# Performance work log

Hardware: AMD Instinct MI355X
Metric: run time of the kernel (lower is better)

Reference implementation:

```python
import jax, jax.numpy as jnp
import numpy as np

B, T, F, U, M = 4096, 16, 256, 512, 8
DELTA_T = 0.04

# ln_tau_table: tau = 1, 10^0.5, 10^1.0, ... -> ln(tau) = i * 0.5*ln(10)
LN_TAU = (jnp.arange(M, dtype=jnp.float32) * (0.5 * np.log(10.0))).astype(jnp.float32)
DECAY = jnp.exp(-DELTA_T / (LN_TAU + 1e-7))  # [M]


def setup_inputs() -> dict:
    key = jax.random.key(0)
    ks = jax.random.split(key, 9)
    s = lambda fan_in: 1.0 / np.sqrt(fan_in)
    return {
        "x": jax.random.normal(ks[0], (B, T, F), dtype=jnp.float32),
        "W_r": jax.random.normal(ks[1], (F + U, U * M), dtype=jnp.float32) * s(F + U),
        "b_r": jax.random.normal(ks[2], (U * M,), dtype=jnp.float32) * 0.01,
        "W_q": jax.random.normal(ks[3], (F + U, U), dtype=jnp.float32) * s(F + U),
        "b_q": jax.random.normal(ks[4], (U,), dtype=jnp.float32) * 0.01,
        "W_s": jax.random.normal(ks[5], (F + U, U * M), dtype=jnp.float32) * s(F + U),
        "b_s": jax.random.normal(ks[6], (U * M,), dtype=jnp.float32) * 0.01,
        "W_out": jax.random.normal(ks[7], (U, 3), dtype=jnp.float32) * s(U),
        "b_out": jax.random.normal(ks[8], (3,), dtype=jnp.float32) * 0.01,
    }


def _ctgru_forward(x, W_r, b_r, W_q, b_q, W_s, b_s, W_out, b_out):
    def step(h_hat, x_t):  # h_hat: [B,U,M], x_t: [B,F]
        h = h_hat.sum(axis=2)                              # [B,U]
        fused = jnp.concatenate([x_t, h], axis=1)          # [B,F+U]
        ln_tau_r = (fused @ W_r + b_r).reshape(-1, U, M)   # [B,U,M]
        r_ki = jax.nn.softmax(-jnp.square(ln_tau_r - LN_TAU), axis=2)
        q_in = jnp.concatenate([x_t, jnp.sum(r_ki * h_hat, axis=2)], axis=1)
        q_k = jnp.tanh(q_in @ W_q + b_q)[:, :, None]       # [B,U,1]
        ln_tau_s = (fused @ W_s + b_s).reshape(-1, U, M)
        s_ki = jax.nn.softmax(-jnp.square(ln_tau_s - LN_TAU), axis=2)
        h_next = ((1.0 - s_ki) * h_hat + s_ki * q_k) * DECAY
        return h_next, h_next.sum(axis=2)                  # carry, hidden [B,U]

    h0 = jnp.zeros((x.shape[0], U, M), dtype=x.dtype)
    _, hiddens = jax.lax.scan(step, h0, jnp.swapaxes(x, 0, 1))  # hiddens: [T,B,U]
    outputs = jnp.swapaxes(hiddens, 0, 1)                  # [B,T,U]
    return outputs @ W_out + b_out                         # [B,T,3]


def reference(x, W_r, b_r, W_q, b_q, W_s, b_s, W_out, b_out):
    return _ctgru_forward(x, W_r, b_r, W_q, b_q, W_s, b_s, W_out, b_out)
```

## Files before the change

kernel.cpp:

```cpp
#include <hip/hip_runtime.h>
#include <hip/hip_bf16.h>
#include <math.h>

#define B_   4096
#define T_   16
#define F_   256
#define U_   512
#define M_   8
#define K_   768
#define NRS  4096
#define NC   8192
#define LNT  1.1512925f

#define XPH  32768
#define XPT  1048576
#define HPH  65536
#define BPH  98304
#define QPH  49152

typedef __bf16 bf16_t;
typedef bf16_t bf16x8 __attribute__((ext_vector_type(8)));
typedef bf16_t bf16x4 __attribute__((ext_vector_type(4)));
typedef float  f32x4  __attribute__((ext_vector_type(4)));

__device__ inline void gl_lds16(const void* g, void* lds) {
    __builtin_amdgcn_global_load_lds(
        (const __attribute__((address_space(1))) unsigned int*)g,
        (__attribute__((address_space(3))) unsigned int*)lds, 16, 0, 0);
}

#define VMCNT(n) asm volatile("s_waitcnt vmcnt(" #n ")" ::: "memory")
#define LGKM0()  asm volatile("s_waitcnt lgkmcnt(0)" ::: "memory")
#define BAR()    __builtin_amdgcn_s_barrier()

__device__ inline void stage8(const bf16_t* src, bf16_t* dst, int tid) {
    gl_lds16(src + tid * 8,        (char*)dst + tid * 16);
    gl_lds16(src + tid * 8 + 2048, (char*)dst + tid * 16 + 4096);
}

template <int IS_R>
__global__ __launch_bounds__(256, 4) void gemm_half(
    const bf16_t* __restrict__ xt_t,
    const bf16_t* __restrict__ ht,
    const bf16_t* __restrict__ Bt,
    const float*  __restrict__ biasP,
    const bf16_t* __restrict__ hhat,
    bf16_t* __restrict__ rh,
    bf16_t* __restrict__ sbuf)
{
    __shared__ __attribute__((aligned(16))) bf16_t Ahl[2][4096];
    __shared__ __attribute__((aligned(16))) bf16_t Bhl[2][4096];

    const int tid  = threadIdx.x;
    const int lane = tid & 63;
    const int wave = tid >> 6;

    const int lin = blockIdx.y * 32 + blockIdx.x;
    const int c = lin & 7, q = lin >> 3;
    const int mh = (c >> 1) * 8 + (q & 7);
    const int nh = (c & 1) * 16 + (q >> 3);
    const int m0 = mh * 128;
    const int NH = IS_R ? nh : 32 + nh;

    const int wm = wave >> 1;
    const int wn = wave & 1;
    const int lr = lane & 15;
    const int kq = lane >> 4;

    const bf16_t* xp = xt_t + (size_t)mh * XPH;
    const bf16_t* hp = ht   + (size_t)mh * HPH;
    const bf16_t* bp = Bt   + (size_t)NH * BPH;

    const int aoff = kq * 1024 + (wm * 64 + lr) * 8;
    const int boff = kq * 1024 + (wn * 64 + lr) * 8;

    f32x4 acc[4][4] = {};

    stage8(xp, &Ahl[0][0], tid);
    stage8(bp, &Bhl[0][0], tid);
    VMCNT(0);
    BAR();

#pragma unroll
    for (int tt = 0; tt < 24; ++tt) {
        const int p = tt & 1, pn = p ^ 1;
        if (tt < 23) {
            const bf16_t* as = (tt + 1 < 8) ? xp + (tt + 1) * 4096
                                            : hp + (tt + 1 - 8) * 4096;
            stage8(as, &Ahl[pn][0], tid);
            stage8(bp + (tt + 1) * 4096, &Bhl[pn][0], tid);
        }
        bf16x8 a[4], b[4];
#pragma unroll
        for (int i = 0; i < 4; ++i)
            a[i] = *(const bf16x8*)(&Ahl[p][0] + aoff + i * 128);
#pragma unroll
        for (int j = 0; j < 4; ++j)
            b[j] = *(const bf16x8*)(&Bhl[p][0] + boff + j * 128);
        LGKM0();
        __builtin_amdgcn_s_setprio(1);
#pragma unroll
        for (int i = 0; i < 4; ++i)
#pragma unroll
            for (int j = 0; j < 4; ++j)
                acc[i][j] = __builtin_amdgcn_mfma_f32_16x16x32_bf16(
                    a[i], b[j], acc[i][j], 0, 0, 0);
        __builtin_amdgcn_s_setprio(0);
        VMCNT(0);
        BAR();
    }

    const int nb  = NH * 128 + wn * 64;
    const int u3  = lane & 7;
    const int m0v = ((lane >> 3) & 1) * 4;

    float bj4[4];
#pragma unroll
    for (int j = 0; j < 4; ++j) bj4[j] = biasP[nb + j * 16 + lr];

#pragma unroll
    for (int mi = 0; mi < 4; ++mi) {
        const int rowb = m0 + wm * 64 + mi * 16 + kq * 4;
#pragma unroll
        for (int r = 0; r < 4; ++r) {
            const int row = rowb + r;
            float e[4], sum = 0.f;
#pragma unroll
            for (int j = 0; j < 4; ++j) {
                float v = acc[mi][j][r] + bj4[j];
                float d = v - (float)(m0v + j) * LNT;
                e[j] = __expf(-d * d);
                sum += e[j];
            }
            sum += __shfl_xor(sum, 8, 64);
            const float inv = 1.0f / sum;
            if (IS_R) {
                bf16x4 h4 = *(const bf16x4*)(hhat + (size_t)row * NRS + nb + u3 * 8 + m0v);
                float rhv = 0.f;
#pragma unroll
                for (int j = 0; j < 4; ++j) rhv += e[j] * inv * (float)h4[j];
                rhv += __shfl_xor(rhv, 8, 64);
                if ((lane & 8) == 0)
                    rh[(size_t)row * U_ + (nb >> 3) + u3] = (bf16_t)rhv;
            } else {
                bf16x4 pv;
#pragma unroll
                for (int j = 0; j < 4; ++j) pv[j] = (bf16_t)(e[j] * inv);
                *(bf16x4*)(sbuf + (size_t)row * NRS + (nb - NRS) + u3 * 8 + m0v) = pv;
            }
        }
    }
}

__global__ __launch_bounds__(256) void gemm_q_up(
    const bf16_t* __restrict__ xt_t,
    const bf16_t* __restrict__ rh,
    const bf16_t* __restrict__ Bqt,
    const float*  __restrict__ bq,
    const bf16_t* __restrict__ sbuf,
    bf16_t* __restrict__ hhat,
    bf16_t* __restrict__ hnext,
    bf16_t* __restrict__ htile)
{
    __shared__ __attribute__((aligned(16))) bf16_t As[4096];
    __shared__ __attribute__((aligned(16))) bf16_t Bs[4096];

    const int tid  = threadIdx.x;
    const int lane = tid & 63;
    const int wave = tid >> 6;
    const int m0 = blockIdx.x * 64;
    const int n0 = blockIdx.y * 64;
    const int wm = wave & 1;
    const int wn = wave >> 1;
    const int lr = lane & 15;
    const int kq = lane >> 4;

    const int chs = (tid >> 6) & 3;
    const int rws = tid & 63;

    const bf16_t* xp  = xt_t + (size_t)(m0 >> 7) * XPH;
    const int     r0  = m0 & 127;
    const bf16_t* bpq = Bqt + (size_t)(n0 >> 6) * QPH;

    f32x4 acc[2][2] = {};

    for (int kt = 0; kt < 12; ++kt) {
        __syncthreads();
        if (kt < 4) {
            gl_lds16(xp + ((size_t)((kt * 2 + 0) * 4 + chs) * 128 + r0 + rws) * 8,
                     (char*)As + tid * 16);
            gl_lds16(xp + ((size_t)((kt * 2 + 1) * 4 + chs) * 128 + r0 + rws) * 8,
                     (char*)As + tid * 16 + 4096);
        } else {
            const int cb = (kt - 4) * 64;
            gl_lds16(rh + (size_t)(m0 + rws) * U_ + cb + chs * 8,
                     (char*)As + tid * 16);
            gl_lds16(rh + (size_t)(m0 + rws) * U_ + cb + 32 + chs * 8,
                     (char*)As + tid * 16 + 4096);
        }
        gl_lds16(bpq + ((size_t)((kt * 2 + 0) * 4 + chs) * 64 + rws) * 8,
                 (char*)Bs + tid * 16);
        gl_lds16(bpq + ((size_t)((kt * 2 + 1) * 4 + chs) * 64 + rws) * 8,
                 (char*)Bs + tid * 16 + 4096);
        __syncthreads();

        bf16x8 af[4], bfr[4];
#pragma unroll
        for (int ks = 0; ks < 2; ks++)
#pragma unroll
            for (int i = 0; i < 2; i++) {
                af[i * 2 + ks]  = *(const bf16x8*)(As +
                    ((ks * 4 + kq) * 64 + wm * 32 + i * 16 + lr) * 8);
                bfr[i * 2 + ks] = *(const bf16x8*)(Bs +
                    ((ks * 4 + kq) * 64 + wn * 32 + i * 16 + lr) * 8);
            }
#pragma unroll
        for (int ks = 0; ks < 2; ks++)
#pragma unroll
            for (int i = 0; i < 2; i++)
#pragma unroll
                for (int j = 0; j < 2; j++)
                    acc[i][j] = __builtin_amdgcn_mfma_f32_16x16x32_bf16(
                        af[i * 2 + ks], bfr[j * 2 + ks], acc[i][j], 0, 0, 0);
    }

    const float DEC[8] = {0.0f, 0.9658531f, 0.9827783f, 0.9884856f,
                          0.9913518f, 0.9930754f, 0.9942261f, 0.9950489f};

#pragma unroll
    for (int i = 0; i < 2; i++) {
        const int rowb = m0 + wm * 32 + i * 16 + kq * 4;
#pragma unroll
        for (int j = 0; j < 2; j++) {
            const int u = n0 + wn * 32 + j * 16 + lr;
            const float bv = bq[u];
#pragma unroll
            for (int r = 0; r < 4; r++) {
                const int row = rowb + r;
                const float qv = tanhf(acc[i][j][r] + bv);
                const size_t base = (size_t)row * NRS + u * 8;
                bf16x8 s8 = *(const bf16x8*)(sbuf + base);
                bf16x8 h8 = *(const bf16x8*)(hhat + base);
                bf16x8 ho;
                float hs = 0.f;
#pragma unroll
                for (int m = 0; m < 8; m++) {
                    float s = (float)s8[m];
                    float h = (float)h8[m];
                    float hn = ((1.f - s) * h + s * qv) * DEC[m];
                    ho[m] = (bf16_t)hn;
                    hs += hn;
                }
                *(bf16x8*)(hhat + base) = ho;
                hnext[(size_t)row * U_ + u] = (bf16_t)hs;
                htile[((size_t)(row >> 7) * 16 + (u >> 5)) * 4096
                      + ((((u >> 3) & 3) * 128) + (row & 127)) * 8 + (u & 7)] = (bf16_t)hs;
            }
        }
    }
}

__global__ void transpose_perm(const float* __restrict__ src, bf16_t* __restrict__ dst) {
    __shared__ float tl[32][33];
    int k0 = blockIdx.x * 32, n0 = blockIdx.y * 32;
    int tx = threadIdx.x & 31, ty = threadIdx.x >> 5;
#pragma unroll
    for (int i = 0; i < 32; i += 8)
        tl[ty + i][tx] = src[(size_t)(k0 + ty + i) * NRS + n0 + tx];
    __syncthreads();
#pragma unroll
    for (int i = 0; i < 32; i += 8) {
        int n = n0 + ty + i;
        int m = n & 7, u3v = (n >> 3) & 7;
        int p = (n & ~63) + (m & 3) * 16 + (m >> 2) * 8 + u3v;
        dst[(size_t)p * K_ + k0 + tx] = (bf16_t)tl[tx][ty + i];
    }
}

__global__ void btile_build(const bf16_t* __restrict__ WrsT, bf16_t* __restrict__ Bt) {
    int n = blockIdx.x / 3;
    int k = (blockIdx.x % 3) * 256 + threadIdx.x;
    int NH = n >> 7, prow = n & 127;
    int kt = k >> 5, ch = (k >> 3) & 3, e = k & 7;
    Bt[(size_t)NH * BPH + (((size_t)kt * 4 + ch) * 128 + prow) * 8 + e]
        = WrsT[(size_t)n * K_ + k];
}

__global__ void transpose_plain(const float* __restrict__ src, bf16_t* __restrict__ dst, int N) {
    __shared__ float tl[32][33];
    int k0 = blockIdx.x * 32, n0 = blockIdx.y * 32;
    int tx = threadIdx.x & 31, ty = threadIdx.x >> 5;
#pragma unroll
    for (int i = 0; i < 32; i += 8)
        tl[ty + i][tx] = src[(size_t)(k0 + ty + i) * N + n0 + tx];
    __syncthreads();
#pragma unroll
    for (int i = 0; i < 32; i += 8)
        dst[(size_t)(n0 + ty + i) * K_ + k0 + tx] = (bf16_t)tl[tx][ty + i];
}

__global__ void bqtile_build(const bf16_t* __restrict__ WqT, bf16_t* __restrict__ Bqt) {
    int n = blockIdx.x / 3;
    int k = (blockIdx.x % 3) * 256 + threadIdx.x;
    int np = n >> 6, prow = n & 63;
    int kt = k >> 5, ch = (k >> 3) & 3, e = k & 7;
    Bqt[(size_t)np * QPH + (((size_t)kt * 4 + ch) * 64 + prow) * 8 + e]
        = WqT[(size_t)n * K_ + k];
}

__global__ void bias_perm(const float* __restrict__ b_r, const float* __restrict__ b_s,
                          float* __restrict__ biasP) {
    int p = blockIdx.x * 256 + threadIdx.x;
    int pr = p & 63, j = pr >> 4, lr = pr & 15;
    int L = (p & ~63) + (lr & 7) * 8 + ((lr >> 3) & 1) * 4 + j;
    biasP[p] = (L < NRS) ? b_r[L] : b_s[L - NRS];
}

__global__ void xtile_build(const float* __restrict__ x, bf16_t* __restrict__ xt) {
    int idx = blockIdx.x * 256 + threadIdx.x;
    int b = idx >> 12;
    int rem = idx & 4095;
    int t = rem >> 8, f = rem & 255;
    int mh = b >> 7, prow = b & 127;
    int kt = f >> 5, ch = (f >> 3) & 3, e = f & 7;
    xt[(size_t)t * XPT + (size_t)mh * XPH
       + (((size_t)kt * 4 + ch) * 128 + prow) * 8 + e] = (bf16_t)x[idx];
}

__global__ __launch_bounds__(256) void out_all(
    const bf16_t* __restrict__ hall,
    const float* __restrict__ Wout,
    const float* __restrict__ bout,
    float* __restrict__ out)
{
    int row = blockIdx.x * 4 + (threadIdx.x >> 6);
    int lane = threadIdx.x & 63;
    bf16x8 h8 = *(const bf16x8*)(hall + (size_t)row * U_ + lane * 8);
    float p0 = 0, p1 = 0, p2 = 0;
#pragma unroll
    for (int k = 0; k < 8; k++) {
        float h = (float)h8[k];
        int u = lane * 8 + k;
        p0 += h * Wout[u * 3 + 0];
        p1 += h * Wout[u * 3 + 1];
        p2 += h * Wout[u * 3 + 2];
    }
    for (int off = 32; off; off >>= 1) {
        p0 += __shfl_down(p0, off, 64);
        p1 += __shfl_down(p1, off, 64);
        p2 += __shfl_down(p2, off, 64);
    }
    if (lane == 0) {
        int t = row >> 12, b = row & (B_ - 1);
        size_t o = ((size_t)b * T_ + t) * 3;
        out[o + 0] = p0 + bout[0];
        out[o + 1] = p1 + bout[1];
        out[o + 2] = p2 + bout[2];
    }
}

extern "C" void kernel_launch(void* const* d_in, const int* in_sizes, int n_in,
                              void* d_out, int out_size, void* d_ws, size_t ws_size,
                              hipStream_t stream) {
    const float* x   = (const float*)d_in[0];
    const float* W_r = (const float*)d_in[1];
    const float* b_r = (const float*)d_in[2];
    const float* W_q = (const float*)d_in[3];
    const float* b_q = (const float*)d_in[4];
    const float* W_s = (const float*)d_in[5];
    const float* b_s = (const float*)d_in[6];
    const float* W_o = (const float*)d_in[7];
    const float* b_o = (const float*)d_in[8];
    float* out = (float*)d_out;

    char* ws = (char*)d_ws;
    bf16_t* hhat  = (bf16_t*)ws; ws += (size_t)B_ * NRS * 2;
    bf16_t* sbuf  = (bf16_t*)ws; ws += (size_t)B_ * NRS * 2;
    bf16_t* xtile = (bf16_t*)ws; ws += (size_t)T_ * XPT * 2;
    bf16_t* hall  = (bf16_t*)ws; ws += (size_t)(T_ + 1) * B_ * U_ * 2;
    bf16_t* rh    = (bf16_t*)ws; ws += (size_t)B_ * U_ * 2;
    bf16_t* WrsT  = (bf16_t*)ws; ws += (size_t)NC * K_ * 2;
    bf16_t* Btile = (bf16_t*)ws; ws += (size_t)NC * K_ * 2;
    bf16_t* htile = (bf16_t*)ws; ws += (size_t)32 * HPH * 2;
    bf16_t* WqT   = (bf16_t*)ws; ws += (size_t)U_ * K_ * 2;
    bf16_t* Bqtil = (bf16_t*)ws; ws += (size_t)8 * QPH * 2;
    float*  biasP = (float*)ws;  ws += (size_t)NC * 4;

    hipMemsetAsync(hhat, 0, (size_t)B_ * NRS * 2, stream);
    hipMemsetAsync(htile, 0, (size_t)32 * HPH * 2, stream);
    xtile_build<<<B_ * T_ * F_ / 256, 256, 0, stream>>>(x, xtile);
    transpose_perm<<<dim3(K_ / 32, NRS / 32), 256, 0, stream>>>(W_r, WrsT);
    transpose_perm<<<dim3(K_ / 32, NRS / 32), 256, 0, stream>>>(W_s, WrsT + (size_t)NRS * K_);
    btile_build<<<NC * 3, 256, 0, stream>>>(WrsT, Btile);
    transpose_plain<<<dim3(K_ / 32, U_ / 32), 256, 0, stream>>>(W_q, WqT, U_);
    bqtile_build<<<U_ * 3, 256, 0, stream>>>(WqT, Bqtil);
    bias_perm<<<NC / 256, 256, 0, stream>>>(b_r, b_s, biasP);

    for (int t = 0; t < T_; t++) {
        const bf16_t* xt_t = xtile + (size_t)t * XPT;
        bf16_t*       hn   = hall + (size_t)(t + 1) * B_ * U_;
        gemm_half<1><<<dim3(32, 32), 256, 0, stream>>>(xt_t, htile, Btile, biasP, hhat, rh, sbuf);
        gemm_half<0><<<dim3(32, 32), 256, 0, stream>>>(xt_t, htile, Btile, biasP, hhat, rh, sbuf);
        gemm_q_up<<<dim3(64, 8), 256, 0, stream>>>(xt_t, rh, Bqtil, b_q, sbuf, hhat, hn, htile);
    }
    out_all<<<B_ * T_ / 4, 256, 0, stream>>>(hall + (size_t)B_ * U_, W_o, b_o, out);
}
```

Baseline: 1.496 ms.

## Merge r/s GEMMs into one launch loading fragments directly from global

```diff
diff --git a/kernel.cpp b/kernel.cpp
--- a/kernel.cpp
+++ b/kernel.cpp
@@ -29,17 +29,7 @@
         (__attribute__((address_space(3))) unsigned int*)lds, 16, 0, 0);
 }
 
-#define VMCNT(n) asm volatile("s_waitcnt vmcnt(" #n ")" ::: "memory")
-#define LGKM0()  asm volatile("s_waitcnt lgkmcnt(0)" ::: "memory")
-#define BAR()    __builtin_amdgcn_s_barrier()
-
-__device__ inline void stage8(const bf16_t* src, bf16_t* dst, int tid) {
-    gl_lds16(src + tid * 8,        (char*)dst + tid * 16);
-    gl_lds16(src + tid * 8 + 2048, (char*)dst + tid * 16 + 4096);
-}
-
-template <int IS_R>
-__global__ __launch_bounds__(256, 4) void gemm_half(
+__global__ __launch_bounds__(256) void gemm_rs_fd(
     const bf16_t* __restrict__ xt_t,
     const bf16_t* __restrict__ ht,
     const bf16_t* __restrict__ Bt,
@@ -48,71 +38,62 @@
     bf16_t* __restrict__ rh,
     bf16_t* __restrict__ sbuf)
 {
-    __shared__ __attribute__((aligned(16))) bf16_t Ahl[2][4096];
-    __shared__ __attribute__((aligned(16))) bf16_t Bhl[2][4096];
-
     const int tid  = threadIdx.x;
     const int lane = tid & 63;
     const int wave = tid >> 6;
 
     const int lin = blockIdx.y * 32 + blockIdx.x;
     const int c = lin & 7, q = lin >> 3;
-    const int mh = (c >> 1) * 8 + (q & 7);
-    const int nh = (c & 1) * 16 + (q >> 3);
+    const int mh = (c >> 2) * 16 + (q & 15);
+    const int NH = (c & 3) * 16 + (q >> 4);
     const int m0 = mh * 128;
-    const int NH = IS_R ? nh : 32 + nh;
 
     const int wm = wave >> 1;
     const int wn = wave & 1;
     const int lr = lane & 15;
     const int kq = lane >> 4;
 
-    const bf16_t* xp = xt_t + (size_t)mh * XPH;
-    const bf16_t* hp = ht   + (size_t)mh * HPH;
-    const bf16_t* bp = Bt   + (size_t)NH * BPH;
+    const bf16_t* apx = xt_t + (size_t)mh * XPH;
+    const bf16_t* aph = ht   + (size_t)mh * HPH;
+    const bf16_t* bp  = Bt   + (size_t)NH * BPH;
 
     const int aoff = kq * 1024 + (wm * 64 + lr) * 8;
     const int boff = kq * 1024 + (wn * 64 + lr) * 8;
 
     f32x4 acc[4][4] = {};
-
-    stage8(xp, &Ahl[0][0], tid);
-    stage8(bp, &Bhl[0][0], tid);
-    VMCNT(0);
-    BAR();
-
-#pragma unroll
-    for (int tt = 0; tt < 24; ++tt) {
-        const int p = tt & 1, pn = p ^ 1;
-        if (tt < 23) {
-            const bf16_t* as = (tt + 1 < 8) ? xp + (tt + 1) * 4096
-                                            : hp + (tt + 1 - 8) * 4096;
-            stage8(as, &Ahl[pn][0], tid);
-            stage8(bp + (tt + 1) * 4096, &Bhl[pn][0], tid);
-        }
-        bf16x8 a[4], b[4];
-#pragma unroll
-        for (int i = 0; i < 4; ++i)
-            a[i] = *(const bf16x8*)(&Ahl[p][0] + aoff + i * 128);
-#pragma unroll
-        for (int j = 0; j < 4; ++j)
-            b[j] = *(const bf16x8*)(&Bhl[p][0] + boff + j * 128);
-        LGKM0();
-        __builtin_amdgcn_s_setprio(1);
-#pragma unroll
-        for (int i = 0; i < 4; ++i)
-#pragma unroll
-            for (int j = 0; j < 4; ++j)
-                acc[i][j] = __builtin_amdgcn_mfma_f32_16x16x32_bf16(
-                    a[i], b[j], acc[i][j], 0, 0, 0);
-        __builtin_amdgcn_s_setprio(0);
-        VMCNT(0);
-        BAR();
-    }
+    bf16x8 a0[4], b0[4], a1[4], b1[4];
+
+#define ABASE(T) ((T) < 8 ? apx + (T) * 4096 : aph + ((T) - 8) * 4096)
+#define LDA(D, T) do{ const bf16_t* _p = ABASE(T) + aoff;                      \
+    D[0] = *(const bf16x8*)(_p);        D[1] = *(const bf16x8*)(_p + 128);     \
+    D[2] = *(const bf16x8*)(_p + 256);  D[3] = *(const bf16x8*)(_p + 384); }while(0)
+#define LDB(D, T) do{ const bf16_t* _p = bp + (T) * 4096 + boff;               \
+    D[0] = *(const bf16x8*)(_p);        D[1] = *(const bf16x8*)(_p + 128);     \
+    D[2] = *(const bf16x8*)(_p + 256);  D[3] = *(const bf16x8*)(_p + 384); }while(0)
+#define MMA(A, B) do{ __builtin_amdgcn_s_setprio(1);                           \
+    _Pragma("unroll") for (int i = 0; i < 4; ++i)                              \
+      _Pragma("unroll") for (int j = 0; j < 4; ++j)                            \
+        acc[i][j] = __builtin_amdgcn_mfma_f32_16x16x32_bf16(                   \
+            A[i], B[j], acc[i][j], 0, 0, 0);                                   \
+    __builtin_amdgcn_s_setprio(0); }while(0)
+
+    LDA(a0, 0); LDB(b0, 0);
+#pragma unroll
+    for (int tt = 0; tt < 24; tt += 2) {
+        if (tt + 1 < 24) { LDA(a1, tt + 1); LDB(b1, tt + 1); }
+        MMA(a0, b0);
+        if (tt + 2 < 24) { LDA(a0, tt + 2); LDB(b0, tt + 2); }
+        MMA(a1, b1);
+    }
+#undef MMA
+#undef LDB
+#undef LDA
+#undef ABASE
 
     const int nb  = NH * 128 + wn * 64;
     const int u3  = lane & 7;
     const int m0v = ((lane >> 3) & 1) * 4;
+    const bool is_r = NH < 32;
 
     float bj4[4];
 #pragma unroll
@@ -134,7 +115,7 @@
             }
             sum += __shfl_xor(sum, 8, 64);
             const float inv = 1.0f / sum;
-            if (IS_R) {
+            if (is_r) {
                 bf16x4 h4 = *(const bf16x4*)(hhat + (size_t)row * NRS + nb + u3 * 8 + m0v);
                 float rhv = 0.f;
 #pragma unroll
@@ -318,13 +299,20 @@
 
 __global__ void xtile_build(const float* __restrict__ x, bf16_t* __restrict__ xt) {
     int idx = blockIdx.x * 256 + threadIdx.x;
-    int b = idx >> 12;
-    int rem = idx & 4095;
-    int t = rem >> 8, f = rem & 255;
+    int b = idx >> 9;
+    int rem = idx & 511;
+    int t = rem >> 5, c8 = rem & 31;
+    int f0 = c8 * 8;
+    const float* src = x + ((size_t)b * T_ + t) * F_ + f0;
+    float4 v0 = *(const float4*)(src);
+    float4 v1 = *(const float4*)(src + 4);
+    bf16x8 o;
+    o[0] = (bf16_t)v0.x; o[1] = (bf16_t)v0.y; o[2] = (bf16_t)v0.z; o[3] = (bf16_t)v0.w;
+    o[4] = (bf16_t)v1.x; o[5] = (bf16_t)v1.y; o[6] = (bf16_t)v1.z; o[7] = (bf16_t)v1.w;
     int mh = b >> 7, prow = b & 127;
-    int kt = f >> 5, ch = (f >> 3) & 3, e = f & 7;
-    xt[(size_t)t * XPT + (size_t)mh * XPH
-       + (((size_t)kt * 4 + ch) * 128 + prow) * 8 + e] = (bf16_t)x[idx];
+    int kt = f0 >> 5, ch = (f0 >> 3) & 3;
+    *(bf16x8*)(xt + (size_t)t * XPT + (size_t)mh * XPH
+               + (((size_t)kt * 4 + ch) * 128 + prow) * 8) = o;
 }
 
 __global__ __launch_bounds__(256) void out_all(
@@ -388,7 +376,7 @@
 
     hipMemsetAsync(hhat, 0, (size_t)B_ * NRS * 2, stream);
     hipMemsetAsync(htile, 0, (size_t)32 * HPH * 2, stream);
-    xtile_build<<<B_ * T_ * F_ / 256, 256, 0, stream>>>(x, xtile);
+    xtile_build<<<B_ * T_ * F_ / 8 / 256, 256, 0, stream>>>(x, xtile);
     transpose_perm<<<dim3(K_ / 32, NRS / 32), 256, 0, stream>>>(W_r, WrsT);
     transpose_perm<<<dim3(K_ / 32, NRS / 32), 256, 0, stream>>>(W_s, WrsT + (size_t)NRS * K_);
     btile_build<<<NC * 3, 256, 0, stream>>>(WrsT, Btile);
@@ -399,8 +387,7 @@
     for (int t = 0; t < T_; t++) {
         const bf16_t* xt_t = xtile + (size_t)t * XPT;
         bf16_t*       hn   = hall + (size_t)(t + 1) * B_ * U_;
-        gemm_half<1><<<dim3(32, 32), 256, 0, stream>>>(xt_t, htile, Btile, biasP, hhat, rh, sbuf);
-        gemm_half<0><<<dim3(32, 32), 256, 0, stream>>>(xt_t, htile, Btile, biasP, hhat, rh, sbuf);
+        gemm_rs_fd<<<dim3(32, 64), 256, 0, stream>>>(xt_t, htile, Btile, biasP, hhat, rh, sbuf);
         gemm_q_up<<<dim3(64, 8), 256, 0, stream>>>(xt_t, rh, Bqtil, b_q, sbuf, hhat, hn, htile);
     }
     out_all<<<B_ * T_ / 4, 256, 0, stream>>>(hall + (size_t)B_ * U_, W_o, b_o, out);
```

Result: slower. 1.823 ms (+21.8%).

## Fuse s-gate GEMM with q-gate GEMM and state update; skip h-part at t=0

Applied to the files above, without the earlier changes.

```diff
diff --git a/kernel.cpp b/kernel.cpp
--- a/kernel.cpp
+++ b/kernel.cpp
@@ -16,7 +16,7 @@
 #define XPT  1048576
 #define HPH  65536
 #define BPH  98304
-#define QPH  49152
+#define QPP  12288
 
 typedef __bf16 bf16_t;
 typedef bf16_t bf16x8 __attribute__((ext_vector_type(8)));
@@ -38,15 +38,13 @@
     gl_lds16(src + tid * 8 + 2048, (char*)dst + tid * 16 + 4096);
 }
 
-template <int IS_R>
-__global__ __launch_bounds__(256, 4) void gemm_half(
+__global__ __launch_bounds__(256, 4) void gemm_r(
     const bf16_t* __restrict__ xt_t,
     const bf16_t* __restrict__ ht,
     const bf16_t* __restrict__ Bt,
     const float*  __restrict__ biasP,
     const bf16_t* __restrict__ hhat,
-    bf16_t* __restrict__ rh,
-    bf16_t* __restrict__ sbuf)
+    bf16_t* __restrict__ rh)
 {
     __shared__ __attribute__((aligned(16))) bf16_t Ahl[2][4096];
     __shared__ __attribute__((aligned(16))) bf16_t Bhl[2][4096];
@@ -60,7 +58,7 @@
     const int mh = (c >> 1) * 8 + (q & 7);
     const int nh = (c & 1) * 16 + (q >> 3);
     const int m0 = mh * 128;
-    const int NH = IS_R ? nh : 32 + nh;
+    const int NH = nh;
 
     const int wm = wave >> 1;
     const int wn = wave & 1;
@@ -134,127 +132,202 @@
             }
             sum += __shfl_xor(sum, 8, 64);
             const float inv = 1.0f / sum;
-            if (IS_R) {
-                bf16x4 h4 = *(const bf16x4*)(hhat + (size_t)row * NRS + nb + u3 * 8 + m0v);
-                float rhv = 0.f;
-#pragma unroll
-                for (int j = 0; j < 4; ++j) rhv += e[j] * inv * (float)h4[j];
-                rhv += __shfl_xor(rhv, 8, 64);
-                if ((lane & 8) == 0)
-                    rh[(size_t)row * U_ + (nb >> 3) + u3] = (bf16_t)rhv;
-            } else {
-                bf16x4 pv;
-#pragma unroll
-                for (int j = 0; j < 4; ++j) pv[j] = (bf16_t)(e[j] * inv);
-                *(bf16x4*)(sbuf + (size_t)row * NRS + (nb - NRS) + u3 * 8 + m0v) = pv;
-            }
-        }
-    }
-}
-
-__global__ __launch_bounds__(256) void gemm_q_up(
+            bf16x4 h4 = *(const bf16x4*)(hhat + (size_t)row * NRS + nb + u3 * 8 + m0v);
+            float rhv = 0.f;
+#pragma unroll
+            for (int j = 0; j < 4; ++j) rhv += e[j] * inv * (float)h4[j];
+            rhv += __shfl_xor(rhv, 8, 64);
+            if ((lane & 8) == 0)
+                rh[(size_t)row * U_ + (nb >> 3) + u3] = (bf16_t)rhv;
+        }
+    }
+}
+
+template <int FIRST>
+__global__ __launch_bounds__(256, 4) void gemm_sq(
     const bf16_t* __restrict__ xt_t,
+    const bf16_t* __restrict__ htr,
+    const bf16_t* __restrict__ Bt,
+    const float*  __restrict__ biasP,
     const bf16_t* __restrict__ rh,
-    const bf16_t* __restrict__ Bqt,
+    const bf16_t* __restrict__ Bq16,
     const float*  __restrict__ bq,
-    const bf16_t* __restrict__ sbuf,
     bf16_t* __restrict__ hhat,
     bf16_t* __restrict__ hnext,
-    bf16_t* __restrict__ htile)
+    bf16_t* __restrict__ htw)
 {
-    __shared__ __attribute__((aligned(16))) bf16_t As[4096];
-    __shared__ __attribute__((aligned(16))) bf16_t Bs[4096];
+    __shared__ __attribute__((aligned(16))) bf16_t Ahl[2][4096];
+    __shared__ __attribute__((aligned(16))) bf16_t Bhl[2][4096];
+    __shared__ __attribute__((aligned(16))) float  qls[2048];
 
     const int tid  = threadIdx.x;
     const int lane = tid & 63;
     const int wave = tid >> 6;
-    const int m0 = blockIdx.x * 64;
-    const int n0 = blockIdx.y * 64;
-    const int wm = wave & 1;
-    const int wn = wave >> 1;
+
+    const int lin = blockIdx.y * 32 + blockIdx.x;
+    const int c = lin & 7, qq = lin >> 3;
+    const int mh = (c >> 1) * 8 + (qq & 7);
+    const int nh = (c & 1) * 16 + (qq >> 3);
+    const int m0 = mh * 128;
+    const int NH = 32 + nh;
+
+    const int wm = wave >> 1;
+    const int wn = wave & 1;
     const int lr = lane & 15;
     const int kq = lane >> 4;
 
-    const int chs = (tid >> 6) & 3;
-    const int rws = tid & 63;
-
-    const bf16_t* xp  = xt_t + (size_t)(m0 >> 7) * XPH;
-    const int     r0  = m0 & 127;
-    const bf16_t* bpq = Bqt + (size_t)(n0 >> 6) * QPH;
-
-    f32x4 acc[2][2] = {};
-
-    for (int kt = 0; kt < 12; ++kt) {
-        __syncthreads();
-        if (kt < 4) {
-            gl_lds16(xp + ((size_t)((kt * 2 + 0) * 4 + chs) * 128 + r0 + rws) * 8,
-                     (char*)As + tid * 16);
-            gl_lds16(xp + ((size_t)((kt * 2 + 1) * 4 + chs) * 128 + r0 + rws) * 8,
-                     (char*)As + tid * 16 + 4096);
-        } else {
-            const int cb = (kt - 4) * 64;
-            gl_lds16(rh + (size_t)(m0 + rws) * U_ + cb + chs * 8,
-                     (char*)As + tid * 16);
-            gl_lds16(rh + (size_t)(m0 + rws) * U_ + cb + 32 + chs * 8,
-                     (char*)As + tid * 16 + 4096);
-        }
-        gl_lds16(bpq + ((size_t)((kt * 2 + 0) * 4 + chs) * 64 + rws) * 8,
-                 (char*)Bs + tid * 16);
-        gl_lds16(bpq + ((size_t)((kt * 2 + 1) * 4 + chs) * 64 + rws) * 8,
-                 (char*)Bs + tid * 16 + 4096);
-        __syncthreads();
-
-        bf16x8 af[4], bfr[4];
-#pragma unroll
-        for (int ks = 0; ks < 2; ks++)
-#pragma unroll
-            for (int i = 0; i < 2; i++) {
-                af[i * 2 + ks]  = *(const bf16x8*)(As +
-                    ((ks * 4 + kq) * 64 + wm * 32 + i * 16 + lr) * 8);
-                bfr[i * 2 + ks] = *(const bf16x8*)(Bs +
-                    ((ks * 4 + kq) * 64 + wn * 32 + i * 16 + lr) * 8);
+    const bf16_t* xp = xt_t + (size_t)mh * XPH;
+    const bf16_t* hp = htr  + (size_t)mh * HPH;
+    const bf16_t* bp = Bt   + (size_t)NH * BPH;
+    const bf16_t* bqp = Bq16 + (size_t)nh * QPP;
+
+    const int NT = FIRST ? 8 : 24;
+
+    {
+        bf16_t* bslab = &Bhl[0][0];
+        f32x4 accq[2] = {};
+
+        const int rws = tid & 127, chs = tid >> 7;
+
+#define STAGE_AQ(KT, DST) do{                                                  \
+        if ((KT) < 8) stage8(xp + (KT) * 4096, DST, tid);                      \
+        else {                                                                 \
+            const int cb_ = ((KT) - 8) * 32;                                   \
+            gl_lds16(rh + (size_t)(m0 + rws) * U_ + cb_ + chs * 8,             \
+                     (char*)(DST) + tid * 16);                                 \
+            gl_lds16(rh + (size_t)(m0 + rws) * U_ + cb_ + 16 + chs * 8,        \
+                     (char*)(DST) + tid * 16 + 4096);                          \
+        } }while(0)
+#define STAGE_BQ(KT, P) do{ if (wave == 0)                                     \
+        gl_lds16(bqp + (KT) * 512 + lane * 8,                                  \
+                 (char*)bslab + (P) * 1024 + lane * 16); }while(0)
+
+        STAGE_AQ(0, &Ahl[0][0]);
+        STAGE_BQ(0, 0);
+        VMCNT(0);
+        BAR();
+#pragma unroll
+        for (int kt = 0; kt < NT; ++kt) {
+            const int p = kt & 1, pn = p ^ 1;
+            if (kt < NT - 1) { STAGE_AQ(kt + 1, &Ahl[pn][0]); STAGE_BQ(kt + 1, pn); }
+            bf16x8 aq[2], bqf;
+#pragma unroll
+            for (int i = 0; i < 2; ++i)
+                aq[i] = *(const bf16x8*)(&Ahl[p][0] + kq * 1024
+                                         + (wave * 32 + i * 16 + lr) * 8);
+            bqf = *(const bf16x8*)(bslab + p * 512 + (kq * 16 + lr) * 8);
+            LGKM0();
+#pragma unroll
+            for (int i = 0; i < 2; ++i)
+                accq[i] = __builtin_amdgcn_mfma_f32_16x16x32_bf16(
+                    aq[i], bqf, accq[i], 0, 0, 0);
+            VMCNT(0);
+            BAR();
+        }
+#undef STAGE_AQ
+#undef STAGE_BQ
+
+        const float bqv = bq[nh * 16 + lr];
+#pragma unroll
+        for (int i = 0; i < 2; ++i)
+#pragma unroll
+            for (int r = 0; r < 4; ++r)
+                qls[(wave * 32 + i * 16 + kq * 4 + r) * 16 + lr] =
+                    tanhf(accq[i][r] + bqv);
+        BAR();
+    }
+
+    const int aoff = kq * 1024 + (wm * 64 + lr) * 8;
+    const int boff = kq * 1024 + (wn * 64 + lr) * 8;
+
+    f32x4 acc[4][4] = {};
+
+    stage8(xp, &Ahl[0][0], tid);
+    stage8(bp, &Bhl[0][0], tid);
+    VMCNT(0);
+    BAR();
+
+#pragma unroll
+    for (int tt = 0; tt < NT; ++tt) {
+        const int p = tt & 1, pn = p ^ 1;
+        if (tt < NT - 1) {
+            const bf16_t* as = (tt + 1 < 8) ? xp + (tt + 1) * 4096
+                                            : hp + (tt + 1 - 8) * 4096;
+            stage8(as, &Ahl[pn][0], tid);
+            stage8(bp + (tt + 1) * 4096, &Bhl[pn][0], tid);
+        }
+        bf16x8 a[4], b[4];
+#pragma unroll
+        for (int i = 0; i < 4; ++i)
+            a[i] = *(const bf16x8*)(&Ahl[p][0] + aoff + i * 128);
+#pragma unroll
+        for (int j = 0; j < 4; ++j)
+            b[j] = *(const bf16x8*)(&Bhl[p][0] + boff + j * 128);
+        LGKM0();
+        __builtin_amdgcn_s_setprio(1);
+#pragma unroll
+        for (int i = 0; i < 4; ++i)
+#pragma unroll
+            for (int j = 0; j < 4; ++j)
+                acc[i][j] = __builtin_amdgcn_mfma_f32_16x16x32_bf16(
+                    a[i], b[j], acc[i][j], 0, 0, 0);
+        __builtin_amdgcn_s_setprio(0);
+        VMCNT(0);
+        BAR();
+    }
+
+    const int nb  = NH * 128 + wn * 64;
+    const int u3  = lane & 7;
+    const int m0v = ((lane >> 3) & 1) * 4;
+    const int hcol = nh * 128 + wn * 64;
+
+    const float DECL[4] = {0.0f, 0.9658531f, 0.9827783f, 0.9884856f};
+    const float DECH[4] = {0.9913518f, 0.9930754f, 0.9942261f, 0.9950489f};
+
+    float bj4[4];
+#pragma unroll
+    for (int j = 0; j < 4; ++j) bj4[j] = biasP[nb + j * 16 + lr];
+
+#pragma unroll
+    for (int mi = 0; mi < 4; ++mi) {
+        const int rowb = m0 + wm * 64 + mi * 16 + kq * 4;
+        const int rlb  = wm * 64 + mi * 16 + kq * 4;
+#pragma unroll
+        for (int r = 0; r < 4; ++r) {
+            const int row = rowb + r;
+            float e[4], sum = 0.f;
+#pragma unroll
+            for (int j = 0; j < 4; ++j) {
+                float v = acc[mi][j][r] + bj4[j];
+                float d = v - (float)(m0v + j) * LNT;
+                e[j] = __expf(-d * d);
+                sum += e[j];
             }
-#pragma unroll
-        for (int ks = 0; ks < 2; ks++)
-#pragma unroll
-            for (int i = 0; i < 2; i++)
-#pragma unroll
-                for (int j = 0; j < 2; j++)
-                    acc[i][j] = __builtin_amdgcn_mfma_f32_16x16x32_bf16(
-                        af[i * 2 + ks], bfr[j * 2 + ks], acc[i][j], 0, 0, 0);
-    }
-
-    const float DEC[8] = {0.0f, 0.9658531f, 0.9827783f, 0.9884856f,
-                          0.9913518f, 0.9930754f, 0.9942261f, 0.9950489f};
-
-#pragma unroll
-    for (int i = 0; i < 2; i++) {
-        const int rowb = m0 + wm * 32 + i * 16 + kq * 4;
-#pragma unroll
-        for (int j = 0; j < 2; j++) {
-            const int u = n0 + wn * 32 + j * 16 + lr;
-            const float bv = bq[u];
-#pragma unroll
-            for (int r = 0; r < 4; r++) {
-                const int row = rowb + r;
-                const float qv = tanhf(acc[i][j][r] + bv);
-                const size_t base = (size_t)row * NRS + u * 8;
-                bf16x8 s8 = *(const bf16x8*)(sbuf + base);
-                bf16x8 h8 = *(const bf16x8*)(hhat + base);
-                bf16x8 ho;
-                float hs = 0.f;
-#pragma unroll
-                for (int m = 0; m < 8; m++) {
-                    float s = (float)s8[m];
-                    float h = (float)h8[m];
-                    float hn = ((1.f - s) * h + s * qv) * DEC[m];
-                    ho[m] = (bf16_t)hn;
-                    hs += hn;
-                }
-                *(bf16x8*)(hhat + base) = ho;
+            sum += __shfl_xor(sum, 8, 64);
+            const float inv = 1.0f / sum;
+            const float qv = qls[(rlb + r) * 16 + wn * 8 + u3];
+
+            const size_t ha = (size_t)row * NRS + hcol + u3 * 8 + m0v;
+            bf16x4 h4;
+            if (!FIRST) h4 = *(const bf16x4*)(hhat + ha);
+            bf16x4 ho;
+            float hs = 0.f;
+#pragma unroll
+            for (int j = 0; j < 4; ++j) {
+                float s = e[j] * inv;
+                float h = FIRST ? 0.f : (float)h4[j];
+                float dec = m0v ? DECH[j] : DECL[j];
+                float hn = ((1.f - s) * h + s * qv) * dec;
+                ho[j] = (bf16_t)hn;
+                hs += hn;
+            }
+            *(bf16x4*)(hhat + ha) = ho;
+            hs += __shfl_xor(hs, 8, 64);
+            if ((lane & 8) == 0) {
+                const int u = nh * 16 + wn * 8 + u3;
                 hnext[(size_t)row * U_ + u] = (bf16_t)hs;
-                htile[((size_t)(row >> 7) * 16 + (u >> 5)) * 4096
-                      + ((((u >> 3) & 3) * 128) + (row & 127)) * 8 + (u & 7)] = (bf16_t)hs;
+                htw[((size_t)(row >> 7) * 16 + (u >> 5)) * 4096
+                    + ((((u >> 3) & 3) * 128) + (row & 127)) * 8 + (u & 7)] = (bf16_t)hs;
             }
         }
     }
@@ -286,26 +359,12 @@
         = WrsT[(size_t)n * K_ + k];
 }
 
-__global__ void transpose_plain(const float* __restrict__ src, bf16_t* __restrict__ dst, int N) {
-    __shared__ float tl[32][33];
-    int k0 = blockIdx.x * 32, n0 = blockIdx.y * 32;
-    int tx = threadIdx.x & 31, ty = threadIdx.x >> 5;
-#pragma unroll
-    for (int i = 0; i < 32; i += 8)
-        tl[ty + i][tx] = src[(size_t)(k0 + ty + i) * N + n0 + tx];
-    __syncthreads();
-#pragma unroll
-    for (int i = 0; i < 32; i += 8)
-        dst[(size_t)(n0 + ty + i) * K_ + k0 + tx] = (bf16_t)tl[tx][ty + i];
-}
-
-__global__ void bqtile_build(const bf16_t* __restrict__ WqT, bf16_t* __restrict__ Bqt) {
-    int n = blockIdx.x / 3;
-    int k = (blockIdx.x % 3) * 256 + threadIdx.x;
-    int np = n >> 6, prow = n & 63;
+__global__ void bq16_build(const float* __restrict__ Wq, bf16_t* __restrict__ Bq16) {
+    int i = blockIdx.x * 256 + threadIdx.x;
+    int k = i >> 9, u = i & 511;
+    int nh = u >> 4, ul = u & 15;
     int kt = k >> 5, ch = (k >> 3) & 3, e = k & 7;
-    Bqt[(size_t)np * QPH + (((size_t)kt * 4 + ch) * 64 + prow) * 8 + e]
-        = WqT[(size_t)n * K_ + k];
+    Bq16[(size_t)nh * QPP + ((size_t)kt * 4 + ch) * 128 + ul * 8 + e] = (bf16_t)Wq[i];
 }
 
 __global__ void bias_perm(const float* __restrict__ b_r, const float* __restrict__ b_s,
@@ -318,13 +377,20 @@
 
 __global__ void xtile_build(const float* __restrict__ x, bf16_t* __restrict__ xt) {
     int idx = blockIdx.x * 256 + threadIdx.x;
-    int b = idx >> 12;
-    int rem = idx & 4095;
-    int t = rem >> 8, f = rem & 255;
+    int b = idx >> 9;
+    int rem = idx & 511;
+    int t = rem >> 5, c8 = rem & 31;
+    int f0 = c8 * 8;
+    const float* src = x + ((size_t)b * T_ + t) * F_ + f0;
+    float4 v0 = *(const float4*)(src);
+    float4 v1 = *(const float4*)(src + 4);
+    bf16x8 o;
+    o[0] = (bf16_t)v0.x; o[1] = (bf16_t)v0.y; o[2] = (bf16_t)v0.z; o[3] = (bf16_t)v0.w;
+    o[4] = (bf16_t)v1.x; o[5] = (bf16_t)v1.y; o[6] = (bf16_t)v1.z; o[7] = (bf16_t)v1.w;
     int mh = b >> 7, prow = b & 127;
-    int kt = f >> 5, ch = (f >> 3) & 3, e = f & 7;
-    xt[(size_t)t * XPT + (size_t)mh * XPH
-       + (((size_t)kt * 4 + ch) * 128 + prow) * 8 + e] = (bf16_t)x[idx];
+    int kt = f0 >> 5, ch = (f0 >> 3) & 3;
+    *(bf16x8*)(xt + (size_t)t * XPT + (size_t)mh * XPH
+               + (((size_t)kt * 4 + ch) * 128 + prow) * 8) = o;
 }
 
 __global__ __launch_bounds__(256) void out_all(
@@ -375,33 +441,38 @@
 
     char* ws = (char*)d_ws;
     bf16_t* hhat  = (bf16_t*)ws; ws += (size_t)B_ * NRS * 2;
-    bf16_t* sbuf  = (bf16_t*)ws; ws += (size_t)B_ * NRS * 2;
     bf16_t* xtile = (bf16_t*)ws; ws += (size_t)T_ * XPT * 2;
     bf16_t* hall  = (bf16_t*)ws; ws += (size_t)(T_ + 1) * B_ * U_ * 2;
     bf16_t* rh    = (bf16_t*)ws; ws += (size_t)B_ * U_ * 2;
     bf16_t* WrsT  = (bf16_t*)ws; ws += (size_t)NC * K_ * 2;
     bf16_t* Btile = (bf16_t*)ws; ws += (size_t)NC * K_ * 2;
-    bf16_t* htile = (bf16_t*)ws; ws += (size_t)32 * HPH * 2;
-    bf16_t* WqT   = (bf16_t*)ws; ws += (size_t)U_ * K_ * 2;
-    bf16_t* Bqtil = (bf16_t*)ws; ws += (size_t)8 * QPH * 2;
+    bf16_t* htA   = (bf16_t*)ws; ws += (size_t)32 * HPH * 2;
+    bf16_t* htB   = (bf16_t*)ws; ws += (size_t)32 * HPH * 2;
+    bf16_t* Bq16  = (bf16_t*)ws; ws += (size_t)32 * QPP * 2;
     float*  biasP = (float*)ws;  ws += (size_t)NC * 4;
 
-    hipMemsetAsync(hhat, 0, (size_t)B_ * NRS * 2, stream);
-    hipMemsetAsync(htile, 0, (size_t)32 * HPH * 2, stream);
-    xtile_build<<<B_ * T_ * F_ / 256, 256, 0, stream>>>(x, xtile);
+    xtile_build<<<B_ * T_ * F_ / 8 / 256, 256, 0, stream>>>(x, xtile);
     transpose_perm<<<dim3(K_ / 32, NRS / 32), 256, 0, stream>>>(W_r, WrsT);
     transpose_perm<<<dim3(K_ / 32, NRS / 32), 256, 0, stream>>>(W_s, WrsT + (size_t)NRS * K_);
     btile_build<<<NC * 3, 256, 0, stream>>>(WrsT, Btile);
-    transpose_plain<<<dim3(K_ / 32, U_ / 32), 256, 0, stream>>>(W_q, WqT, U_);
-    bqtile_build<<<U_ * 3, 256, 0, stream>>>(WqT, Bqtil);
+    bq16_build<<<K_ * U_ / 256, 256, 0, stream>>>(W_q, Bq16);
     bias_perm<<<NC / 256, 256, 0, stream>>>(b_r, b_s, biasP);
 
+    bf16_t* htbuf[2] = {htA, htB};
     for (int t = 0; t < T_; t++) {
         const bf16_t* xt_t = xtile + (size_t)t * XPT;
+        const bf16_t* htr  = htbuf[t & 1];
+        bf16_t*       htw  = htbuf[(t + 1) & 1];
         bf16_t*       hn   = hall + (size_t)(t + 1) * B_ * U_;
-        gemm_half<1><<<dim3(32, 32), 256, 0, stream>>>(xt_t, htile, Btile, biasP, hhat, rh, sbuf);
-        gemm_half<0><<<dim3(32, 32), 256, 0, stream>>>(xt_t, htile, Btile, biasP, hhat, rh, sbuf);
-        gemm_q_up<<<dim3(64, 8), 256, 0, stream>>>(xt_t, rh, Bqtil, b_q, sbuf, hhat, hn, htile);
+        if (t == 0) {
+            gemm_sq<1><<<dim3(32, 32), 256, 0, stream>>>(
+                xt_t, htr, Btile, biasP, rh, Bq16, b_q, hhat, hn, htw);
+        } else {
+            gemm_r<<<dim3(32, 32), 256, 0, stream>>>(
+                xt_t, htr, Btile, biasP, hhat, rh);
+            gemm_sq<0><<<dim3(32, 32), 256, 0, stream>>>(
+                xt_t, htr, Btile, biasP, rh, Bq16, b_q, hhat, hn, htw);
+        }
     }
     out_all<<<B_ * T_ / 4, 256, 0, stream>>>(hall + (size_t)B_ * U_, W_o, b_o, out);
 }
```

Measured after the change: 1.492 ms. About the same (-0.3%).
